# Kernel optimization log

Hardware: AMD Instinct MI355X
Metric: run time of the kernel (lower is better)

## Reference

```python
import jax, jax.numpy as jnp
import numpy as np

T, D, H, E = 8192, 1024, 512, 8
BLK = 32  # MXFP8 scaling block size along the contraction dim


def setup_inputs() -> dict:
    key = jax.random.key(0)
    k1, k2, k3, k4 = jax.random.split(key, 4)
    # qdata: values representable-ish in e4m3 (we use small normal floats)
    output_e4m3 = jax.random.normal(k1, (T, D), dtype=jnp.float32)
    # e8m0 scales are powers of two, one per 32-element block along dim
    output_scales_e8m0 = jnp.exp2(
        jax.random.randint(k2, (T, D // BLK), -2, 3).astype(jnp.float32)
    )
    # uniform token distribution across experts (tokens are expert-contiguous)
    num_tokens_per_expert = jnp.full((E,), T // E, dtype=jnp.int32)
    expert_padded_offsets = jnp.zeros((E,), dtype=jnp.int32)  # unused by forward body
    w13 = jax.random.normal(k3, (E, 2 * H, D), dtype=jnp.float32) * 0.02
    w2 = jax.random.normal(k4, (E, D, H), dtype=jnp.float32) * 0.02
    return {
        "output_e4m3": output_e4m3,
        "output_scales_e8m0": output_scales_e8m0,
        "num_tokens_per_expert": num_tokens_per_expert,
        "expert_padded_offsets": expert_padded_offsets,
        "w13": w13,
        "w2": w2,
    }


def reference(output_e4m3, output_scales_e8m0, num_tokens_per_expert,
              expert_padded_offsets, w13, w2):
    # Dequantize MXFP8: qdata * per-block e8m0 scale, blocks of 32 along dim.
    scales = jnp.repeat(output_scales_e8m0, BLK, axis=-1)  # [T, D]
    x = output_e4m3 * scales  # [T, D] high-precision reference activations
    # Grouped GEMM 1: tokens are expert-contiguous with uniform group sizes,
    # so the ragged grouped matmul reduces to a batched einsum per expert.
    tpe = T // E
    xg = x.reshape(E, tpe, D)                       # [E, tpe, D]
    h13 = jnp.einsum("etd,ehd->eth", xg, w13)       # [E, tpe, 2H]
    h1, h3 = h13[..., :H], h13[..., H:]
    h = jax.nn.silu(h1) * h3                        # fused SiLU-gate
    # Grouped GEMM 2
    out = jnp.einsum("eth,edh->etd", h, w2)         # [E, tpe, D]
    return out.reshape(T, D)
```

## Files before the change

### kernel.cpp

```cpp
#include <hip/hip_runtime.h>
#include <hip/hip_bf16.h>

#define T_TOK 8192
#define DDIM  1024
#define HDIM  512
#define NE    8
#define TPE   (T_TOK / NE)

typedef __attribute__((ext_vector_type(4))) float floatx4;
typedef __attribute__((ext_vector_type(8))) short bf16x8;

__device__ __forceinline__ unsigned short f2bf(float f) {
    union { float f; unsigned int u; } v;
    v.f = f;
    unsigned int u = v.u;
    unsigned int r = u + 0x7FFFu + ((u >> 16) & 1u);
    return (unsigned short)(r >> 16);
}

__device__ __forceinline__ void gld_lds16(const void* g, void* l) {
    __builtin_amdgcn_global_load_lds(
        (const __attribute__((address_space(1))) unsigned int*)g,
        (__attribute__((address_space(3))) unsigned int*)l, 16, 0, 0);
}

__global__ __launch_bounds__(256)
void convert_kernel(const float* __restrict__ X, const float* __restrict__ S,
                    const float* __restrict__ W13, const float* __restrict__ W2,
                    unsigned short* __restrict__ Xb,
                    unsigned short* __restrict__ W13b,
                    unsigned short* __restrict__ W2b)
{
    const int NTX  = (T_TOK * DDIM) / 4;
    const int NT13 = (NE * 2 * HDIM * DDIM) / 4;
    const int NT2  = (NE * DDIM * HDIM) / 4;
    const int stride = gridDim.x * blockDim.x;
    for (int i = blockIdx.x * blockDim.x + threadIdx.x; i < NTX + NT13 + NT2; i += stride) {
        float4 v;
        ushort4* dst;
        if (i < NTX) {
            int row = i >> 8;
            int c4  = i & 255;
            v = reinterpret_cast<const float4*>(X)[i];
            float sc = S[row * (DDIM / 32) + (c4 >> 3)];
            v.x *= sc; v.y *= sc; v.z *= sc; v.w *= sc;
            dst = (ushort4*)Xb + i;
        } else if (i < NTX + NT13) {
            int j = i - NTX;
            v = reinterpret_cast<const float4*>(W13)[j];
            dst = (ushort4*)W13b + j;
        } else {
            int j = i - NTX - NT13;
            v = reinterpret_cast<const float4*>(W2)[j];
            dst = (ushort4*)W2b + j;
        }
        ushort4 b;
        b.x = f2bf(v.x); b.y = f2bf(v.y); b.z = f2bf(v.z); b.w = f2bf(v.w);
        *dst = b;
    }
}

__device__ __forceinline__ int xcd_swizzle_512(int raw) {
    return (raw & 7) * 64 + (raw >> 3);
}


__global__ __launch_bounds__(256, 2)
void gemm1_silu_kernel(const unsigned short* __restrict__ Xb,
                       const unsigned short* __restrict__ W13b,
                       __hip_bfloat16* __restrict__ Hout)
{
    const int bid = xcd_swizzle_512(blockIdx.x);
    const int e  = bid >> 6;
    const int nt = (bid >> 3) & 7;
    const int mt = bid & 7;
    const int tok0 = e * TPE + mt * 128;
    const unsigned short* __restrict__ We = W13b + (size_t)e * (2 * HDIM) * DDIM;

    __shared__ __hip_bfloat16 sA[2][128][64];
    __shared__ __hip_bfloat16 sB[2][128][64];

    const int tid  = threadIdx.x;
    const int lane = tid & 63;
    const int wave = tid >> 6;
    const int wr = wave >> 1;
    const int wc = wave & 1;
    const int lr = lane & 15;
    const int sw0 = ((lane >> 4) ^ (lane & 7));

    floatx4 acc1[4][2] = {};
    floatx4 acc3[4][2] = {};

    const int srow0 = (tid >> 3);
    const int dcol  = (tid & 7) * 8;
    const int gcol  = ((tid & 7) ^ (srow0 & 7)) * 8;

    auto STAGE = [&](int kk, int buf) {
        const int k0 = kk * 64;
        #pragma unroll
        for (int j = 0; j < 4; ++j) {
            int row = srow0 + j * 32;
            gld_lds16(&Xb[(size_t)(tok0 + row) * DDIM + k0 + gcol],
                      &sA[buf][row][dcol]);
            int wrow = (j < 2) ? (nt * 64 + row)
                               : (HDIM + nt * 64 + (row - 64));
            gld_lds16(&We[(size_t)wrow * DDIM + k0 + gcol],
                      &sB[buf][row][dcol]);
        }
    };
    auto COMPUTE = [&](int buf) {
        #pragma unroll
        for (int ks = 0; ks < 2; ++ks) {
            const int rc = (sw0 ^ (ks << 2)) << 3;
            bf16x8 a[4], b1[2], b3[2];
            #pragma unroll
            for (int m = 0; m < 4; ++m)
                a[m] = *reinterpret_cast<const bf16x8*>(&sA[buf][wr * 64 + m * 16 + lr][rc]);
            #pragma unroll
            for (int n = 0; n < 2; ++n) {
                b1[n] = *reinterpret_cast<const bf16x8*>(&sB[buf][wc * 32 + n * 16 + lr][rc]);
                b3[n] = *reinterpret_cast<const bf16x8*>(&sB[buf][64 + wc * 32 + n * 16 + lr][rc]);
            }
            #pragma unroll
            for (int m = 0; m < 4; ++m)
                #pragma unroll
                for (int n = 0; n < 2; ++n) {
                    acc1[m][n] = __builtin_amdgcn_mfma_f32_16x16x32_bf16(a[m], b1[n], acc1[m][n], 0, 0, 0);
                    acc3[m][n] = __builtin_amdgcn_mfma_f32_16x16x32_bf16(a[m], b3[n], acc3[m][n], 0, 0, 0);
                }
        }
    };

    STAGE(0, 0);
    for (int kk = 0; kk < DDIM / 64 - 1; ++kk) {
        STAGE(kk + 1, (kk + 1) & 1);
        asm volatile("s_waitcnt vmcnt(8)" ::: "memory");
        __builtin_amdgcn_sched_barrier(0);
        __builtin_amdgcn_s_barrier();
        COMPUTE(kk & 1);
        __builtin_amdgcn_s_barrier();
    }
    asm volatile("s_waitcnt vmcnt(0)" ::: "memory");
    __builtin_amdgcn_sched_barrier(0);
    __builtin_amdgcn_s_barrier();
    COMPUTE(1);

    const int hcol0 = nt * 64 + wc * 32;
    #pragma unroll
    for (int m = 0; m < 4; ++m) {
        #pragma unroll
        for (int n = 0; n < 2; ++n) {
            #pragma unroll
            for (int i = 0; i < 4; ++i) {
                int row = tok0 + wr * 64 + m * 16 + (lane >> 4) * 4 + i;
                int col = hcol0 + n * 16 + (lane & 15);
                float h1 = acc1[m][n][i];
                float h3 = acc3[m][n][i];
                float sig = 1.0f / (1.0f + __expf(-h1));
                Hout[(size_t)row * HDIM + col] = __float2bfloat16(h1 * sig * h3);
            }
        }
    }
}

__global__ __launch_bounds__(256, 2)
void gemm2_kernel(const __hip_bfloat16* __restrict__ Hin,
                  const unsigned short* __restrict__ W2b,
                  float* __restrict__ Out)
{
    const int bid = xcd_swizzle_512(blockIdx.x);
    const int e  = bid >> 6;
    const int mt = (bid >> 3) & 7;
    const int nt = bid & 7;
    const int tok0 = e * TPE + mt * 128;
    const unsigned short* __restrict__ We = W2b + (size_t)e * DDIM * HDIM;

    __shared__ __hip_bfloat16 sA[2][128][64];
    __shared__ __hip_bfloat16 sB[2][128][64];

    const int tid  = threadIdx.x;
    const int lane = tid & 63;
    const int wave = tid >> 6;
    const int wr = wave >> 1;
    const int wc = wave & 1;
    const int lr = lane & 15;
    const int sw0 = ((lane >> 4) ^ (lane & 7));

    floatx4 acc[4][4] = {};

    const int srow0 = (tid >> 3);
    const int dcol  = (tid & 7) * 8;
    const int gcol  = ((tid & 7) ^ (srow0 & 7)) * 8;

    auto STAGE = [&](int kk, int buf) {
        const int k0 = kk * 64;
        #pragma unroll
        for (int j = 0; j < 4; ++j) {
            int row = srow0 + j * 32;
            gld_lds16(&Hin[(size_t)(tok0 + row) * HDIM + k0 + gcol],
                      &sA[buf][row][dcol]);
            gld_lds16(&We[(size_t)(nt * 128 + row) * HDIM + k0 + gcol],
                      &sB[buf][row][dcol]);
        }
    };
    auto COMPUTE = [&](int buf) {
        #pragma unroll
        for (int ks = 0; ks < 2; ++ks) {
            const int rc = (sw0 ^ (ks << 2)) << 3;
            bf16x8 a[4], b[4];
            #pragma unroll
            for (int m = 0; m < 4; ++m)
                a[m] = *reinterpret_cast<const bf16x8*>(&sA[buf][wr * 64 + m * 16 + lr][rc]);
            #pragma unroll
            for (int n = 0; n < 4; ++n)
                b[n] = *reinterpret_cast<const bf16x8*>(&sB[buf][wc * 64 + n * 16 + lr][rc]);
            #pragma unroll
            for (int m = 0; m < 4; ++m)
                #pragma unroll
                for (int n = 0; n < 4; ++n)
                    acc[m][n] = __builtin_amdgcn_mfma_f32_16x16x32_bf16(a[m], b[n], acc[m][n], 0, 0, 0);
        }
    };

    STAGE(0, 0);
    for (int kk = 0; kk < HDIM / 64 - 1; ++kk) {
        STAGE(kk + 1, (kk + 1) & 1);
        asm volatile("s_waitcnt vmcnt(8)" ::: "memory");
        __builtin_amdgcn_sched_barrier(0);
        __builtin_amdgcn_s_barrier();
        COMPUTE(kk & 1);
        __builtin_amdgcn_s_barrier();
    }
    asm volatile("s_waitcnt vmcnt(0)" ::: "memory");
    __builtin_amdgcn_sched_barrier(0);
    __builtin_amdgcn_s_barrier();
    COMPUTE(1);

    const int dcol0 = nt * 128 + wc * 64;
    #pragma unroll
    for (int m = 0; m < 4; ++m) {
        #pragma unroll
        for (int n = 0; n < 4; ++n) {
            #pragma unroll
            for (int i = 0; i < 4; ++i) {
                int row = tok0 + wr * 64 + m * 16 + (lane >> 4) * 4 + i;
                int col = dcol0 + n * 16 + (lane & 15);
                Out[(size_t)row * DDIM + col] = acc[m][n][i];
            }
        }
    }
}

extern "C" void kernel_launch(void* const* d_in, const int* in_sizes, int n_in,
                              void* d_out, int out_size, void* d_ws, size_t ws_size,
                              hipStream_t stream) {
    const float* X   = (const float*)d_in[0];
    const float* S   = (const float*)d_in[1];
    const float* W13 = (const float*)d_in[4];
    const float* W2  = (const float*)d_in[5];
    float* Out = (float*)d_out;

    unsigned short* W13b = (unsigned short*)d_ws;
    unsigned short* W2b  = W13b + (size_t)NE * 2 * HDIM * DDIM;
    __hip_bfloat16* Hb   = (__hip_bfloat16*)(W2b + (size_t)NE * DDIM * HDIM);
    unsigned short* Xb   = (unsigned short*)d_out;

    convert_kernel<<<2048, 256, 0, stream>>>(X, S, W13, W2, Xb, W13b, W2b);
    gemm1_silu_kernel<<<NE * 8 * 8, 256, 0, stream>>>(Xb, W13b, Hb);
    gemm2_kernel<<<NE * 8 * 8, 256, 0, stream>>>(Hb, W2b, Out);
}
```

Measured before the change: 59.13 us.

## Fuse X dequant and W2 bf16 conversion into GEMM loaders via registers

Removes the X dequantize-to-bf16 and W2 conversion passes from the standalone convert kernel. GEMM1 now loads fp32 X and scales directly into registers, applies the scale, packs to bf16 with v_cvt_pk_bf16 and writes to swizzled LDS. GEMM2 does the same for fp32 W2. This saves a full round trip of the 32MB X tensor and the W2 tensor through memory. The cost is twice the global read bytes per tile, register staging with more VGPR pressure, and redundant conversion across tiles that share a block. The M/N tile ordering in the grid swizzle is also swapped so that blocks sharing a weight or activation tile sit together.

```diff
diff --git a/kernel.cpp b/kernel.cpp
--- a/kernel.cpp
+++ b/kernel.cpp
@@ -18,6 +18,12 @@
     return (unsigned short)(r >> 16);
 }
 
+__device__ __forceinline__ unsigned int cvt_pk_bf16(float lo, float hi) {
+    unsigned int r;
+    asm("v_cvt_pk_bf16_f32 %0, %1, %2" : "=v"(r) : "v"(lo), "v"(hi));
+    return r;
+}
+
 __device__ __forceinline__ void gld_lds16(const void* g, void* l) {
     __builtin_amdgcn_global_load_lds(
         (const __attribute__((address_space(1))) unsigned int*)g,
@@ -25,38 +31,16 @@
 }
 
 __global__ __launch_bounds__(256)
-void convert_kernel(const float* __restrict__ X, const float* __restrict__ S,
-                    const float* __restrict__ W13, const float* __restrict__ W2,
-                    unsigned short* __restrict__ Xb,
-                    unsigned short* __restrict__ W13b,
-                    unsigned short* __restrict__ W2b)
+void convert_w13_kernel(const float* __restrict__ W13,
+                        unsigned short* __restrict__ W13b)
 {
-    const int NTX  = (T_TOK * DDIM) / 4;
     const int NT13 = (NE * 2 * HDIM * DDIM) / 4;
-    const int NT2  = (NE * DDIM * HDIM) / 4;
     const int stride = gridDim.x * blockDim.x;
-    for (int i = blockIdx.x * blockDim.x + threadIdx.x; i < NTX + NT13 + NT2; i += stride) {
-        float4 v;
-        ushort4* dst;
-        if (i < NTX) {
-            int row = i >> 8;
-            int c4  = i & 255;
-            v = reinterpret_cast<const float4*>(X)[i];
-            float sc = S[row * (DDIM / 32) + (c4 >> 3)];
-            v.x *= sc; v.y *= sc; v.z *= sc; v.w *= sc;
-            dst = (ushort4*)Xb + i;
-        } else if (i < NTX + NT13) {
-            int j = i - NTX;
-            v = reinterpret_cast<const float4*>(W13)[j];
-            dst = (ushort4*)W13b + j;
-        } else {
-            int j = i - NTX - NT13;
-            v = reinterpret_cast<const float4*>(W2)[j];
-            dst = (ushort4*)W2b + j;
-        }
+    for (int i = blockIdx.x * blockDim.x + threadIdx.x; i < NT13; i += stride) {
+        float4 v = reinterpret_cast<const float4*>(W13)[i];
         ushort4 b;
         b.x = f2bf(v.x); b.y = f2bf(v.y); b.z = f2bf(v.z); b.w = f2bf(v.w);
-        *dst = b;
+        reinterpret_cast<ushort4*>(W13b)[i] = b;
     }
 }
 
@@ -66,14 +50,15 @@
 
 
 __global__ __launch_bounds__(256, 2)
-void gemm1_silu_kernel(const unsigned short* __restrict__ Xb,
+void gemm1_silu_kernel(const float* __restrict__ X,
+                       const float* __restrict__ S,
                        const unsigned short* __restrict__ W13b,
                        __hip_bfloat16* __restrict__ Hout)
 {
     const int bid = xcd_swizzle_512(blockIdx.x);
     const int e  = bid >> 6;
-    const int nt = (bid >> 3) & 7;
-    const int mt = bid & 7;
+    const int mt = (bid >> 3) & 7;
+    const int nt = bid & 7;
     const int tok0 = e * TPE + mt * 128;
     const unsigned short* __restrict__ We = W13b + (size_t)e * (2 * HDIM) * DDIM;
 
@@ -92,20 +77,45 @@
     floatx4 acc3[4][2] = {};
 
     const int srow0 = (tid >> 3);
+    const int c8    = (tid & 7) * 8;
     const int dcol  = (tid & 7) * 8;
-    const int gcol  = ((tid & 7) ^ (srow0 & 7)) * 8;
-
-    auto STAGE = [&](int kk, int buf) {
+    const int swcol = ((tid & 7) ^ (srow0 & 7)) * 8;
+
+    float4 rA[8]; float rs[4];
+
+    auto LOADA = [&](int kk) {
         const int k0 = kk * 64;
         #pragma unroll
         for (int j = 0; j < 4; ++j) {
             int row = srow0 + j * 32;
-            gld_lds16(&Xb[(size_t)(tok0 + row) * DDIM + k0 + gcol],
-                      &sA[buf][row][dcol]);
+            const float* p = &X[(size_t)(tok0 + row) * DDIM + k0 + c8];
+            rA[2*j]   = *reinterpret_cast<const float4*>(p);
+            rA[2*j+1] = *reinterpret_cast<const float4*>(p + 4);
+            rs[j] = S[(size_t)(tok0 + row) * (DDIM / 32) + ((k0 + c8) >> 5)];
+        }
+    };
+    auto STAGEB = [&](int kk, int buf) {
+        const int k0 = kk * 64;
+        #pragma unroll
+        for (int j = 0; j < 4; ++j) {
+            int row = srow0 + j * 32;
             int wrow = (j < 2) ? (nt * 64 + row)
                                : (HDIM + nt * 64 + (row - 64));
-            gld_lds16(&We[(size_t)wrow * DDIM + k0 + gcol],
+            gld_lds16(&We[(size_t)wrow * DDIM + k0 + swcol],
                       &sB[buf][row][dcol]);
+        }
+    };
+    auto WRITEA = [&](int buf) {
+        #pragma unroll
+        for (int j = 0; j < 4; ++j) {
+            int row = srow0 + j * 32;
+            float sc = rs[j];
+            uint4 w;
+            w.x = cvt_pk_bf16(rA[2*j].x * sc,   rA[2*j].y * sc);
+            w.y = cvt_pk_bf16(rA[2*j].z * sc,   rA[2*j].w * sc);
+            w.z = cvt_pk_bf16(rA[2*j+1].x * sc, rA[2*j+1].y * sc);
+            w.w = cvt_pk_bf16(rA[2*j+1].z * sc, rA[2*j+1].w * sc);
+            *reinterpret_cast<uint4*>(&sA[buf][row][swcol]) = w;
         }
     };
     auto COMPUTE = [&](int buf) {
@@ -131,16 +141,30 @@
         }
     };
 
-    STAGE(0, 0);
+    LOADA(0);
+    __builtin_amdgcn_sched_barrier(0);
+    STAGEB(0, 0);
+    __builtin_amdgcn_sched_barrier(0);
     for (int kk = 0; kk < DDIM / 64 - 1; ++kk) {
-        STAGE(kk + 1, (kk + 1) & 1);
-        asm volatile("s_waitcnt vmcnt(8)" ::: "memory");
+        const int buf = kk & 1;
+        asm volatile("s_waitcnt vmcnt(4)" ::: "memory");
+        __builtin_amdgcn_sched_barrier(0);
+        WRITEA(buf);
+        __builtin_amdgcn_sched_barrier(0);
+        LOADA(kk + 1);
+        __builtin_amdgcn_sched_barrier(0);
+        STAGEB(kk + 1, buf ^ 1);
+        __builtin_amdgcn_sched_barrier(0);
+        asm volatile("s_waitcnt vmcnt(16) lgkmcnt(0)" ::: "memory");
         __builtin_amdgcn_sched_barrier(0);
         __builtin_amdgcn_s_barrier();
-        COMPUTE(kk & 1);
+        COMPUTE(buf);
         __builtin_amdgcn_s_barrier();
     }
-    asm volatile("s_waitcnt vmcnt(0)" ::: "memory");
+    asm volatile("s_waitcnt vmcnt(4)" ::: "memory");
+    __builtin_amdgcn_sched_barrier(0);
+    WRITEA(1);
+    asm volatile("s_waitcnt vmcnt(0) lgkmcnt(0)" ::: "memory");
     __builtin_amdgcn_sched_barrier(0);
     __builtin_amdgcn_s_barrier();
     COMPUTE(1);
@@ -165,15 +189,15 @@
 
 __global__ __launch_bounds__(256, 2)
 void gemm2_kernel(const __hip_bfloat16* __restrict__ Hin,
-                  const unsigned short* __restrict__ W2b,
+                  const float* __restrict__ W2,
                   float* __restrict__ Out)
 {
     const int bid = xcd_swizzle_512(blockIdx.x);
     const int e  = bid >> 6;
-    const int mt = (bid >> 3) & 7;
-    const int nt = bid & 7;
+    const int nt = (bid >> 3) & 7;
+    const int mt = bid & 7;
     const int tok0 = e * TPE + mt * 128;
-    const unsigned short* __restrict__ We = W2b + (size_t)e * DDIM * HDIM;
+    const float* __restrict__ We = W2 + (size_t)e * DDIM * HDIM;
 
     __shared__ __hip_bfloat16 sA[2][128][64];
     __shared__ __hip_bfloat16 sB[2][128][64];
@@ -189,18 +213,41 @@
     floatx4 acc[4][4] = {};
 
     const int srow0 = (tid >> 3);
+    const int c8    = (tid & 7) * 8;
     const int dcol  = (tid & 7) * 8;
-    const int gcol  = ((tid & 7) ^ (srow0 & 7)) * 8;
-
-    auto STAGE = [&](int kk, int buf) {
+    const int swcol = ((tid & 7) ^ (srow0 & 7)) * 8;
+
+    float4 rB[8];
+
+    auto LOADB = [&](int kk) {
         const int k0 = kk * 64;
         #pragma unroll
         for (int j = 0; j < 4; ++j) {
             int row = srow0 + j * 32;
-            gld_lds16(&Hin[(size_t)(tok0 + row) * HDIM + k0 + gcol],
+            const float* p = &We[(size_t)(nt * 128 + row) * HDIM + k0 + c8];
+            rB[2*j]   = *reinterpret_cast<const float4*>(p);
+            rB[2*j+1] = *reinterpret_cast<const float4*>(p + 4);
+        }
+    };
+    auto STAGEA = [&](int kk, int buf) {
+        const int k0 = kk * 64;
+        #pragma unroll
+        for (int j = 0; j < 4; ++j) {
+            int row = srow0 + j * 32;
+            gld_lds16(&Hin[(size_t)(tok0 + row) * HDIM + k0 + swcol],
                       &sA[buf][row][dcol]);
-            gld_lds16(&We[(size_t)(nt * 128 + row) * HDIM + k0 + gcol],
-                      &sB[buf][row][dcol]);
+        }
+    };
+    auto WRITEB = [&](int buf) {
+        #pragma unroll
+        for (int j = 0; j < 4; ++j) {
+            int row = srow0 + j * 32;
+            uint4 w;
+            w.x = cvt_pk_bf16(rB[2*j].x,   rB[2*j].y);
+            w.y = cvt_pk_bf16(rB[2*j].z,   rB[2*j].w);
+            w.z = cvt_pk_bf16(rB[2*j+1].x, rB[2*j+1].y);
+            w.w = cvt_pk_bf16(rB[2*j+1].z, rB[2*j+1].w);
+            *reinterpret_cast<uint4*>(&sB[buf][row][swcol]) = w;
         }
     };
     auto COMPUTE = [&](int buf) {
@@ -222,16 +269,30 @@
         }
     };
 
-    STAGE(0, 0);
+    LOADB(0);
+    __builtin_amdgcn_sched_barrier(0);
+    STAGEA(0, 0);
+    __builtin_amdgcn_sched_barrier(0);
     for (int kk = 0; kk < HDIM / 64 - 1; ++kk) {
-        STAGE(kk + 1, (kk + 1) & 1);
-        asm volatile("s_waitcnt vmcnt(8)" ::: "memory");
+        const int buf = kk & 1;
+        asm volatile("s_waitcnt vmcnt(4)" ::: "memory");
+        __builtin_amdgcn_sched_barrier(0);
+        WRITEB(buf);
+        __builtin_amdgcn_sched_barrier(0);
+        LOADB(kk + 1);
+        __builtin_amdgcn_sched_barrier(0);
+        STAGEA(kk + 1, buf ^ 1);
+        __builtin_amdgcn_sched_barrier(0);
+        asm volatile("s_waitcnt vmcnt(12) lgkmcnt(0)" ::: "memory");
         __builtin_amdgcn_sched_barrier(0);
         __builtin_amdgcn_s_barrier();
-        COMPUTE(kk & 1);
+        COMPUTE(buf);
         __builtin_amdgcn_s_barrier();
     }
-    asm volatile("s_waitcnt vmcnt(0)" ::: "memory");
+    asm volatile("s_waitcnt vmcnt(4)" ::: "memory");
+    __builtin_amdgcn_sched_barrier(0);
+    WRITEB(1);
+    asm volatile("s_waitcnt vmcnt(0) lgkmcnt(0)" ::: "memory");
     __builtin_amdgcn_sched_barrier(0);
     __builtin_amdgcn_s_barrier();
     COMPUTE(1);
@@ -261,11 +322,9 @@
     float* Out = (float*)d_out;
 
     unsigned short* W13b = (unsigned short*)d_ws;
-    unsigned short* W2b  = W13b + (size_t)NE * 2 * HDIM * DDIM;
-    __hip_bfloat16* Hb   = (__hip_bfloat16*)(W2b + (size_t)NE * DDIM * HDIM);
-    unsigned short* Xb   = (unsigned short*)d_out;
-
-    convert_kernel<<<2048, 256, 0, stream>>>(X, S, W13, W2, Xb, W13b, W2b);
-    gemm1_silu_kernel<<<NE * 8 * 8, 256, 0, stream>>>(Xb, W13b, Hb);
-    gemm2_kernel<<<NE * 8 * 8, 256, 0, stream>>>(Hb, W2b, Out);
-}
+    __hip_bfloat16* Hb   = (__hip_bfloat16*)(W13b + (size_t)NE * 2 * HDIM * DDIM);
+
+    convert_w13_kernel<<<2048, 256, 0, stream>>>(W13, W13b);
+    gemm1_silu_kernel<<<NE * 8 * 8, 256, 0, stream>>>(X, S, W13b, Hb);
+    gemm2_kernel<<<NE * 8 * 8, 256, 0, stream>>>(Hb, W2, Out);
+}
```

Measured after the change: 58.05 us. Within noise of the previous version (-1.8%).

## Fuse W2 fp32-to-bf16 conversion into gemm2 B-tile staging via registers

Applied to the files above, without the earlier changes.

The separate conversion pass over W2 is removed from the convert kernel. gemm2 now loads fp32 W2 tiles into registers, converts them with packed bf16 instructions, and writes them swizzled into LDS, using a rebalanced vmcnt/lgkmcnt pipeline. This saves one full write and re-read of W2 in bf16. In exchange gemm2 reads twice the bytes for B and uses more registers. The block-index mapping of mt/nt is also swapped in both GEMMs, changing which tiles share an XCD.

```diff
diff --git a/kernel.cpp b/kernel.cpp
--- a/kernel.cpp
+++ b/kernel.cpp
@@ -18,6 +18,12 @@
     return (unsigned short)(r >> 16);
 }
 
+__device__ __forceinline__ unsigned int cvt_pk_bf16(float lo, float hi) {
+    unsigned int r;
+    asm("v_cvt_pk_bf16_f32 %0, %1, %2" : "=v"(r) : "v"(lo), "v"(hi));
+    return r;
+}
+
 __device__ __forceinline__ void gld_lds16(const void* g, void* l) {
     __builtin_amdgcn_global_load_lds(
         (const __attribute__((address_space(1))) unsigned int*)g,
@@ -26,16 +32,14 @@
 
 __global__ __launch_bounds__(256)
 void convert_kernel(const float* __restrict__ X, const float* __restrict__ S,
-                    const float* __restrict__ W13, const float* __restrict__ W2,
+                    const float* __restrict__ W13,
                     unsigned short* __restrict__ Xb,
-                    unsigned short* __restrict__ W13b,
-                    unsigned short* __restrict__ W2b)
+                    unsigned short* __restrict__ W13b)
 {
     const int NTX  = (T_TOK * DDIM) / 4;
     const int NT13 = (NE * 2 * HDIM * DDIM) / 4;
-    const int NT2  = (NE * DDIM * HDIM) / 4;
     const int stride = gridDim.x * blockDim.x;
-    for (int i = blockIdx.x * blockDim.x + threadIdx.x; i < NTX + NT13 + NT2; i += stride) {
+    for (int i = blockIdx.x * blockDim.x + threadIdx.x; i < NTX + NT13; i += stride) {
         float4 v;
         ushort4* dst;
         if (i < NTX) {
@@ -45,14 +49,10 @@
             float sc = S[row * (DDIM / 32) + (c4 >> 3)];
             v.x *= sc; v.y *= sc; v.z *= sc; v.w *= sc;
             dst = (ushort4*)Xb + i;
-        } else if (i < NTX + NT13) {
+        } else {
             int j = i - NTX;
             v = reinterpret_cast<const float4*>(W13)[j];
             dst = (ushort4*)W13b + j;
-        } else {
-            int j = i - NTX - NT13;
-            v = reinterpret_cast<const float4*>(W2)[j];
-            dst = (ushort4*)W2b + j;
         }
         ushort4 b;
         b.x = f2bf(v.x); b.y = f2bf(v.y); b.z = f2bf(v.z); b.w = f2bf(v.w);
@@ -72,8 +72,8 @@
 {
     const int bid = xcd_swizzle_512(blockIdx.x);
     const int e  = bid >> 6;
-    const int nt = (bid >> 3) & 7;
-    const int mt = bid & 7;
+    const int mt = (bid >> 3) & 7;
+    const int nt = bid & 7;
     const int tok0 = e * TPE + mt * 128;
     const unsigned short* __restrict__ We = W13b + (size_t)e * (2 * HDIM) * DDIM;
 
@@ -165,15 +165,15 @@
 
 __global__ __launch_bounds__(256, 2)
 void gemm2_kernel(const __hip_bfloat16* __restrict__ Hin,
-                  const unsigned short* __restrict__ W2b,
+                  const float* __restrict__ W2,
                   float* __restrict__ Out)
 {
     const int bid = xcd_swizzle_512(blockIdx.x);
     const int e  = bid >> 6;
-    const int mt = (bid >> 3) & 7;
-    const int nt = bid & 7;
+    const int nt = (bid >> 3) & 7;
+    const int mt = bid & 7;
     const int tok0 = e * TPE + mt * 128;
-    const unsigned short* __restrict__ We = W2b + (size_t)e * DDIM * HDIM;
+    const float* __restrict__ We = W2 + (size_t)e * DDIM * HDIM;
 
     __shared__ __hip_bfloat16 sA[2][128][64];
     __shared__ __hip_bfloat16 sB[2][128][64];
@@ -189,18 +189,41 @@
     floatx4 acc[4][4] = {};
 
     const int srow0 = (tid >> 3);
+    const int c8    = (tid & 7) * 8;
     const int dcol  = (tid & 7) * 8;
-    const int gcol  = ((tid & 7) ^ (srow0 & 7)) * 8;
-
-    auto STAGE = [&](int kk, int buf) {
+    const int swcol = ((tid & 7) ^ (srow0 & 7)) * 8;
+
+    float4 rB[8];
+
+    auto LOADB = [&](int kk) {
         const int k0 = kk * 64;
         #pragma unroll
         for (int j = 0; j < 4; ++j) {
             int row = srow0 + j * 32;
-            gld_lds16(&Hin[(size_t)(tok0 + row) * HDIM + k0 + gcol],
+            const float* p = &We[(size_t)(nt * 128 + row) * HDIM + k0 + c8];
+            rB[2*j]   = *reinterpret_cast<const float4*>(p);
+            rB[2*j+1] = *reinterpret_cast<const float4*>(p + 4);
+        }
+    };
+    auto STAGEA = [&](int kk, int buf) {
+        const int k0 = kk * 64;
+        #pragma unroll
+        for (int j = 0; j < 4; ++j) {
+            int row = srow0 + j * 32;
+            gld_lds16(&Hin[(size_t)(tok0 + row) * HDIM + k0 + swcol],
                       &sA[buf][row][dcol]);
-            gld_lds16(&We[(size_t)(nt * 128 + row) * HDIM + k0 + gcol],
-                      &sB[buf][row][dcol]);
+        }
+    };
+    auto WRITEB = [&](int buf) {
+        #pragma unroll
+        for (int j = 0; j < 4; ++j) {
+            int row = srow0 + j * 32;
+            uint4 w;
+            w.x = cvt_pk_bf16(rB[2*j].x,   rB[2*j].y);
+            w.y = cvt_pk_bf16(rB[2*j].z,   rB[2*j].w);
+            w.z = cvt_pk_bf16(rB[2*j+1].x, rB[2*j+1].y);
+            w.w = cvt_pk_bf16(rB[2*j+1].z, rB[2*j+1].w);
+            *reinterpret_cast<uint4*>(&sB[buf][row][swcol]) = w;
         }
     };
     auto COMPUTE = [&](int buf) {
@@ -222,16 +245,30 @@
         }
     };
 
-    STAGE(0, 0);
+    LOADB(0);
+    __builtin_amdgcn_sched_barrier(0);
+    STAGEA(0, 0);
+    __builtin_amdgcn_sched_barrier(0);
     for (int kk = 0; kk < HDIM / 64 - 1; ++kk) {
-        STAGE(kk + 1, (kk + 1) & 1);
-        asm volatile("s_waitcnt vmcnt(8)" ::: "memory");
+        const int buf = kk & 1;
+        asm volatile("s_waitcnt vmcnt(4)" ::: "memory");
+        __builtin_amdgcn_sched_barrier(0);
+        WRITEB(buf);
+        __builtin_amdgcn_sched_barrier(0);
+        LOADB(kk + 1);
+        __builtin_amdgcn_sched_barrier(0);
+        STAGEA(kk + 1, buf ^ 1);
+        __builtin_amdgcn_sched_barrier(0);
+        asm volatile("s_waitcnt vmcnt(12) lgkmcnt(0)" ::: "memory");
         __builtin_amdgcn_sched_barrier(0);
         __builtin_amdgcn_s_barrier();
-        COMPUTE(kk & 1);
+        COMPUTE(buf);
         __builtin_amdgcn_s_barrier();
     }
-    asm volatile("s_waitcnt vmcnt(0)" ::: "memory");
+    asm volatile("s_waitcnt vmcnt(4)" ::: "memory");
+    __builtin_amdgcn_sched_barrier(0);
+    WRITEB(1);
+    asm volatile("s_waitcnt vmcnt(0) lgkmcnt(0)" ::: "memory");
     __builtin_amdgcn_sched_barrier(0);
     __builtin_amdgcn_s_barrier();
     COMPUTE(1);
@@ -261,11 +298,10 @@
     float* Out = (float*)d_out;
 
     unsigned short* W13b = (unsigned short*)d_ws;
-    unsigned short* W2b  = W13b + (size_t)NE * 2 * HDIM * DDIM;
-    __hip_bfloat16* Hb   = (__hip_bfloat16*)(W2b + (size_t)NE * DDIM * HDIM);
+    __hip_bfloat16* Hb   = (__hip_bfloat16*)(W13b + (size_t)NE * 2 * HDIM * DDIM);
     unsigned short* Xb   = (unsigned short*)d_out;
 
-    convert_kernel<<<2048, 256, 0, stream>>>(X, S, W13, W2, Xb, W13b, W2b);
+    convert_kernel<<<2048, 256, 0, stream>>>(X, S, W13, Xb, W13b);
     gemm1_silu_kernel<<<NE * 8 * 8, 256, 0, stream>>>(Xb, W13b, Hb);
-    gemm2_kernel<<<NE * 8 * 8, 256, 0, stream>>>(Hb, W2b, Out);
-}
+    gemm2_kernel<<<NE * 8 * 8, 256, 0, stream>>>(Hb, W2, Out);
+}
```

After: 57.59 us. 2.6% less time.
